# Kernel optimization log

Measured on AMD Instinct MI355X. Metric: run time of the kernel, lower is better.

## Reference

```python
import jax, jax.numpy as jnp
import numpy as np

EPS = 1e-5
INC1, INC2 = 256, 256
MIDC1, MIDC2 = INC1 // 4, INC2 // 4  # 64, 64
B, H, W = 4, 64, 64


def _bn_eval(x, w, b, m, v):
    # x: (B, C, H, W); inference-mode BatchNorm2d
    inv = w / jnp.sqrt(v + EPS)
    return x * inv[None, :, None, None] + (b - m * inv)[None, :, None, None]


def setup_inputs() -> dict:
    key = jax.random.key(0)
    ks = jax.random.split(key, 24)
    f32 = jnp.float32
    d = {
        'fusion': jax.random.normal(ks[0], (B, INC1, H, W), f32),
        'input_rgb': jax.random.normal(ks[1], (B, INC1, H, W), f32),
        'input_dsm': jax.random.normal(ks[2], (B, INC2, H, W), f32),
        # BatchNorm2d params (eval mode: running stats)
        'bn1_w': jax.random.normal(ks[3], (INC1,), f32) * 0.1 + 1.0,
        'bn1_b': jax.random.normal(ks[4], (INC1,), f32) * 0.1,
        'bn1_m': jax.random.normal(ks[5], (INC1,), f32) * 0.1,
        'bn1_v': jax.random.uniform(ks[6], (INC1,), f32, 0.5, 1.5),
        'bn2_w': jax.random.normal(ks[7], (INC2,), f32) * 0.1 + 1.0,
        'bn2_b': jax.random.normal(ks[8], (INC2,), f32) * 0.1,
        'bn2_m': jax.random.normal(ks[9], (INC2,), f32) * 0.1,
        'bn2_v': jax.random.uniform(ks[10], (INC2,), f32, 0.5, 1.5),
        # Linear layers: weight is (out, in) like torch
        'kq1_w': jax.random.normal(ks[11], (2 * MIDC2, INC1), f32) * 0.02,
        'kq1_b': jnp.zeros((2 * MIDC2,), f32),
        'kq2_w': jax.random.normal(ks[12], (2 * MIDC2, INC2), f32) * 0.02,
        'kq2_b': jnp.zeros((2 * MIDC2,), f32),
        'v_w': jax.random.normal(ks[13], (2 * MIDC1, INC1), f32) * 0.02,
        'v_b': jnp.zeros((2 * MIDC1,), f32),
        'out_w': jax.random.normal(ks[14], (INC1, 2 * MIDC1), f32) * 0.02,
        'out_b': jnp.zeros((INC1,), f32),
        'bnl_w': jax.random.normal(ks[15], (INC1,), f32) * 0.1 + 1.0,
        'bnl_b': jax.random.normal(ks[16], (INC1,), f32) * 0.1,
        'bnl_m': jax.random.normal(ks[17], (INC1,), f32) * 0.1,
        'bnl_v': jax.random.uniform(ks[18], (INC1,), f32, 0.5, 1.5),
        'gamma': jax.random.normal(ks[19], (1,), f32) * 0.1,
    }
    return d


def reference(fusion, input_rgb, input_dsm,
              bn1_w, bn1_b, bn1_m, bn1_v,
              bn2_w, bn2_b, bn2_m, bn2_v,
              kq1_w, kq1_b, kq2_w, kq2_b,
              v_w, v_b, out_w, out_b,
              bnl_w, bnl_b, bnl_m, bnl_v, gamma):
    b, _, h, w = fusion.shape
    N = h * w
    rgb = _bn_eval(input_rgb, bn1_w, bn1_b, bn1_m, bn1_v)
    dsm = _bn_eval(input_dsm, bn2_w, bn2_b, bn2_m, bn2_v)
    # flatten NCHW -> (B, N, C)
    rgb_t = rgb.transpose(0, 2, 3, 1).reshape(b, N, -1)
    dsm_t = dsm.transpose(0, 2, 3, 1).reshape(b, N, -1)
    kq1 = rgb_t @ kq1_w.T + kq1_b  # (B, N, 2*MIDC2)
    kq2 = dsm_t @ kq2_w.T + kq2_b  # (B, N, 2*MIDC2)
    # channel shuffle with groups=2: interleave kq1/kq2 channels
    kq = jnp.stack([kq1, kq2], axis=-1).reshape(b, N, 4 * MIDC2)
    k1 = kq[..., 0 * MIDC2:1 * MIDC2]
    q1 = kq[..., 1 * MIDC2:2 * MIDC2]
    k2 = kq[..., 2 * MIDC2:3 * MIDC2]
    q2 = kq[..., 3 * MIDC2:4 * MIDC2]
    fus_t = fusion.transpose(0, 2, 3, 1).reshape(b, N, -1)
    vproj = fus_t @ v_w.T + v_b  # (B, N, 2*MIDC1)
    v1 = vproj[..., :MIDC1]
    v2 = vproj[..., MIDC1:]
    scale = 1.0 / jnp.sqrt(jnp.float32(MIDC2))
    # branch 1: naive softmax attention (dropout is identity at eval)
    a1 = jax.nn.softmax(jnp.einsum('bnd,bmd->bnm', q1, k1) * scale, axis=-1)
    o1 = jnp.einsum('bnm,bmd->bnd', a1, v1)
    # branch 2
    a2 = jax.nn.softmax(jnp.einsum('bnd,bmd->bnm', q2, k2) * scale, axis=-1)
    o2 = jnp.einsum('bnm,bmd->bnd', a2, v2)
    o = jnp.concatenate([o1, o2], axis=-1).reshape(b, h, w, 2 * MIDC1)
    o = o @ out_w.T + out_b  # (B, H, W, INC1)
    o = o.transpose(0, 3, 1, 2)  # (B, INC1, H, W)
    o = _bn_eval(o, bnl_w, bnl_b, bnl_m, bnl_v)
    out = jax.nn.sigmoid(o) * fusion * gamma + fusion
    return out
```

## Files before the change

kernel.cpp:

```cpp
#include <hip/hip_runtime.h>

typedef __bf16 bf16;
typedef __bf16 bf16x8 __attribute__((ext_vector_type(8)));
typedef float f32x2 __attribute__((ext_vector_type(2)));
typedef float f32x4 __attribute__((ext_vector_type(4)));
typedef float f32x16 __attribute__((ext_vector_type(16)));
typedef unsigned int u32;
typedef u32 u32x2 __attribute__((ext_vector_type(2)));
typedef u32 u32x4 __attribute__((ext_vector_type(4)));

#define MFMA16(A,B,C) __builtin_amdgcn_mfma_f32_16x16x32_bf16(A,B,C,0,0,0)
#define MFMA32(A,B,C) __builtin_amdgcn_mfma_f32_32x32x16_bf16(A,B,C,0,0,0)

#define ALPHA 0.18033688f
#define LOG2E 1.44269504f

static __device__ __forceinline__ u32 cvt_pk_bf16(float lo, float hi) {
    u32 r;
    asm("v_cvt_pk_bf16_f32 %0, %1, %2" : "=v"(r) : "v"(lo), "v"(hi));
    return r;
}
static __device__ __forceinline__ void permlane32_swap(u32& a, u32& b) {
    asm("v_permlane32_swap_b32 %0, %1" : "+v"(a), "+v"(b));
}
static __device__ __forceinline__ float vexp2(float x) {
    float r;
    asm("v_exp_f32 %0, %1" : "=v"(r) : "v"(x));
    return r;
}
static __device__ __forceinline__ float vrcp(float x) {
    float r;
    asm("v_rcp_f32 %0, %1" : "=v"(r) : "v"(x));
    return r;
}
static __device__ __forceinline__ void stage16(const bf16* g, bf16* l) {
    __builtin_amdgcn_global_load_lds(
        (const __attribute__((address_space(1))) void*)g,
        (__attribute__((address_space(3))) void*)l, 16, 0, 0);
}

__global__ __launch_bounds__(64) void wprep_kernel(
    const float* __restrict__ kq1w, const float* __restrict__ kq1b,
    const float* __restrict__ bn1w, const float* __restrict__ bn1b,
    const float* __restrict__ bn1m, const float* __restrict__ bn1v,
    const float* __restrict__ kq2w, const float* __restrict__ kq2b,
    const float* __restrict__ bn2w, const float* __restrict__ bn2b,
    const float* __restrict__ bn2m, const float* __restrict__ bn2v,
    const float* __restrict__ vw,   const float* __restrict__ vb,
    const float* __restrict__ outw, const float* __restrict__ outb,
    const float* __restrict__ bnlw, const float* __restrict__ bnlb,
    const float* __restrict__ bnlm, const float* __restrict__ bnlv,
    bf16* __restrict__ Wk1, bf16* __restrict__ Wk2, bf16* __restrict__ Wv,
    bf16* __restrict__ Wo,
    float* __restrict__ B1, float* __restrict__ B2, float* __restrict__ Bv,
    float* __restrict__ Bo)
{
    const int blk = blockIdx.x, lane = threadIdx.x;
    if (blk < 384) {
        const int arr = blk >> 7, j = blk & 127;
        const float* W  = arr == 0 ? kq1w : arr == 1 ? kq2w : vw;
        const float* bs = arr == 0 ? kq1b : arr == 1 ? kq2b : vb;
        bf16*  Wd = arr == 0 ? Wk1 : arr == 1 ? Wk2 : Wv;
        float* Bd = arr == 0 ? B1  : arr == 1 ? B2  : Bv;
        const float scale = (arr < 2 && ((j >> 5) & 1)) ? ALPHA : 1.0f;
        const int c0 = lane * 4;
        f32x4 w4 = *(const f32x4*)(W + j * 256 + c0);
        f32x4 o4; float dot = 0.f;
        if (arr < 2) {
            const float* bw = arr ? bn2w : bn1w;
            const float* bb = arr ? bn2b : bn1b;
            const float* bm = arr ? bn2m : bn1m;
            const float* bv = arr ? bn2v : bn1v;
            f32x4 gw = *(const f32x4*)(bw + c0), gb = *(const f32x4*)(bb + c0);
            f32x4 gm = *(const f32x4*)(bm + c0), gv = *(const f32x4*)(bv + c0);
#pragma unroll
            for (int k = 0; k < 4; ++k) {
                float iv = gw[k] * rsqrtf(gv[k] + 1e-5f);
                float beta = gb[k] - gm[k] * iv;
                o4[k] = w4[k] * iv * scale;
                dot += w4[k] * beta;
            }
        } else {
#pragma unroll
            for (int k = 0; k < 4; ++k) o4[k] = w4[k];
        }
        u32x2 pk; pk[0] = cvt_pk_bf16(o4[0], o4[1]); pk[1] = cvt_pk_bf16(o4[2], o4[3]);
        *(u32x2*)(Wd + j * 256 + c0) = pk;
#pragma unroll
        for (int off = 32; off >= 1; off >>= 1) dot += __shfl_xor(dot, off);
        if (lane == 0) Bd[j] = (bs[j] + dot) * scale;
    } else {
        const int c = blk - 384;
        const float iv = bnlw[c] * rsqrtf(bnlv[c] + 1e-5f);
        const int k0 = lane * 2;
        f32x2 w2 = *(const f32x2*)(outw + c * 128 + k0);
        *(u32*)(Wo + c * 128 + k0) = cvt_pk_bf16(w2[0] * iv, w2[1] * iv);
        if (lane == 0) Bo[c] = outb[c] * iv + bnlb[c] - bnlm[c] * iv;
    }
}

__global__ __launch_bounds__(256) void prep_kernel(
    const float* __restrict__ rgb, const float* __restrict__ dsm,
    const float* __restrict__ fus,
    const bf16* __restrict__ Wk1, const bf16* __restrict__ Wk2,
    const bf16* __restrict__ Wv,
    const float* __restrict__ B1, const float* __restrict__ B2,
    const float* __restrict__ Bv,
    bf16* __restrict__ Kp, bf16* __restrict__ Q, bf16* __restrict__ Vp)
{
    __shared__ __align__(16) float sX[256][34];

    const int id = blockIdx.x;
    const int mode = id >> 9, sub = id & 511;
    const int b = sub >> 7, nt = sub & 127;
    const int t = threadIdx.x;

    const float* X  = mode == 0 ? rgb : mode == 1 ? dsm : fus;
    const bf16*  W  = mode == 0 ? Wk1 : mode == 1 ? Wk2 : Wv;
    const float* Bs = mode == 0 ? B1  : mode == 1 ? B2  : Bv;

    const float* Xb = X + (size_t)b * 1048576 + (size_t)nt * 32;

#pragma unroll
    for (int i = 0; i < 8; ++i) {
        const int chunk = i * 256 + t;
        const int c = chunk >> 3, nn4 = (chunk & 7) * 4;
        const f32x4 v4 = *(const f32x4*)(Xb + (size_t)c * 4096 + nn4);
        *(f32x4*)(&sX[c][nn4]) = v4;
    }
    __syncthreads();

    const int lane = t & 63, w = t >> 6;
    const int l15 = lane & 15, g = lane >> 4;
    const int nloc = (w & 1) * 16 + l15;
    const int n = nt * 32 + nloc;
    const int cibase = (w >> 1) * 4;

    const f32x4 z4 = {0.f, 0.f, 0.f, 0.f};
    f32x4 acc[4] = {z4, z4, z4, z4};

#pragma unroll
    for (int ks = 0; ks < 8; ++ks) {
        const int c0 = ks * 32 + g * 8;
        u32x4 xb;
#pragma unroll
        for (int pr = 0; pr < 4; ++pr)
            xb[pr] = cvt_pk_bf16(sX[c0 + 2 * pr][nloc], sX[c0 + 2 * pr + 1][nloc]);
        const bf16x8 bfr = __builtin_bit_cast(bf16x8, xb);
#pragma unroll
        for (int ci = 0; ci < 4; ++ci) {
            bf16x8 af = *(const bf16x8*)(W + ((cibase + ci) * 16 + l15) * 256 + c0);
            acc[ci] = MFMA16(af, bfr, acc[ci]);
        }
    }

#pragma unroll
    for (int ci = 0; ci < 4; ++ci) {
        const int cia = cibase + ci;
        const int j0 = cia * 16 + g * 4;
        const f32x4 bq = *(const f32x4*)(Bs + j0);
        float v0 = acc[ci][0] + bq[0], v1 = acc[ci][1] + bq[1];
        float v2 = acc[ci][2] + bq[2], v3 = acc[ci][3] + bq[3];
        if (mode == 2) {
            const int head = cia >> 2;
            const int bh = b * 2 + head;
            const int dbase = (cia & 3) * 16 + g * 4;
            const int kbg = n >> 6, key = n & 63;
            const int kc = key >> 4, hi2 = (key >> 3) & 1, inner = key & 7;
            bf16* vp = Vp + (size_t)(bh * 64 + kbg) * 4096;
            const float vv[4] = {v0, v1, v2, v3};
#pragma unroll
            for (int rr = 0; rr < 4; ++rr) {
                const int d = dbase + rr;
                const int chunk = (((d >> 5) * 4 + kc) * 2 + hi2) * 32 + (d & 31);
                vp[chunk * 8 + inner] = (bf16)vv[rr];
            }
        } else {
            const int seg = cia >> 1;
            const int head = seg >> 1;
            const int bh = b * 2 + head;
            const int d0 = (cia & 1) * 16 + g * 4 + (mode == 1 ? 32 : 0);
            u32x2 pk; pk[0] = cvt_pk_bf16(v0, v1); pk[1] = cvt_pk_bf16(v2, v3);
            if (seg & 1) {
                *(u32x2*)(Q + ((size_t)bh * 4096 + n) * 64 + d0) = pk;
            } else {
                const int kbg = n >> 6, r = n & 63;
                const int chunk = (((r >> 5) * 4 + (d0 >> 4)) * 2 + ((d0 >> 3) & 1)) * 32 + (r & 31);
                *(u32x2*)(Kp + (size_t)(bh * 64 + kbg) * 4096 + chunk * 8 + (d0 & 7)) = pk;
            }
        }
    }
}

__global__ __launch_bounds__(512) void attn_kernel(
    const bf16* __restrict__ Kp, const bf16* __restrict__ Q,
    const bf16* __restrict__ Vp,
    bf16* __restrict__ Opart, float* __restrict__ Ml)
{
    __shared__ __align__(16) bf16 sK[2][4096];
    __shared__ __align__(16) bf16 sV[2][4096];

    const int id = blockIdx.x;
    const int bh = id & 7;
    const int qt = (id >> 3) & 15;
    const int s  = id >> 7;

    const int t = threadIdx.x, lane = t & 63, w = t >> 6;
    const int l31 = lane & 31, hi = lane >> 5;
    const int qrow = qt * 256 + w * 32 + l31;
    const int base = bh * 4096;

    bf16x8 qf[4];
    {
        const bf16* qp = Q + ((size_t)(base + qrow)) * 64 + hi * 8;
#pragma unroll
        for (int ds = 0; ds < 4; ++ds) qf[ds] = *(const bf16x8*)(qp + ds * 16);
    }

    f32x16 ot0, ot1;
#pragma unroll
    for (int i = 0; i < 16; ++i) { ot0[i] = 0.f; ot1[i] = 0.f; }
    float lsum = 0.f;

    const bf16* Kblk = Kp + (size_t)(bh * 64 + s * 16) * 4096;
    const bf16* Vblk = Vp + (size_t)(bh * 64 + s * 16) * 4096;
    const int wo = w * 512 + lane * 8;

#define STAGE(BUF, KBI)                                                      \
    {                                                                        \
        const size_t gb = (size_t)(KBI) * 4096 + wo;                         \
        stage16(Kblk + gb, &sK[BUF][w * 512]);                               \
        stage16(Vblk + gb, &sV[BUF][w * 512]);                               \
    }

    STAGE(0, 0);
    __syncthreads();
    int buf = 0;

    for (int kb = 0; kb < 16; ++kb) {
        if (kb + 1 < 16) {
            if (buf) STAGE(0, kb + 1) else STAGE(1, kb + 1);
        }
        const bf16* Kl = &sK[buf][0];
        const bf16* Vl = &sV[buf][0];

        bf16x8 pa[4];
#pragma unroll
        for (int kt = 0; kt < 2; ++kt) {
            f32x16 a;
#pragma unroll
            for (int i = 0; i < 16; ++i) a[i] = 0.f;
#pragma unroll
            for (int ds = 0; ds < 4; ++ds)
                a = MFMA32(*(const bf16x8*)(Kl + (kt * 4 + ds) * 512 + lane * 8), qf[ds], a);
#pragma unroll
            for (int r = 0; r < 16; ++r) a[r] = vexp2(a[r]);
            lsum += (((a[0] + a[1]) + (a[2] + a[3])) +
                     ((a[4] + a[5]) + (a[6] + a[7]))) +
                    (((a[8] + a[9]) + (a[10] + a[11])) +
                     ((a[12] + a[13]) + (a[14] + a[15])));
            u32 wa0 = cvt_pk_bf16(a[0], a[1]);
            u32 wa1 = cvt_pk_bf16(a[2], a[3]);
            u32 wb0 = cvt_pk_bf16(a[4], a[5]);
            u32 wb1 = cvt_pk_bf16(a[6], a[7]);
            permlane32_swap(wa0, wb0);
            permlane32_swap(wa1, wb1);
            u32x4 pk0; pk0[0] = wa0; pk0[1] = wa1; pk0[2] = wb0; pk0[3] = wb1;
            pa[2 * kt] = __builtin_bit_cast(bf16x8, pk0);
            u32 wc0 = cvt_pk_bf16(a[8], a[9]);
            u32 wc1 = cvt_pk_bf16(a[10], a[11]);
            u32 wd0 = cvt_pk_bf16(a[12], a[13]);
            u32 wd1 = cvt_pk_bf16(a[14], a[15]);
            permlane32_swap(wc0, wd0);
            permlane32_swap(wc1, wd1);
            u32x4 pk1; pk1[0] = wc0; pk1[1] = wc1; pk1[2] = wd0; pk1[3] = wd1;
            pa[2 * kt + 1] = __builtin_bit_cast(bf16x8, pk1);
        }
#pragma unroll
        for (int ks = 0; ks < 4; ++ks)
            ot0 = MFMA32(*(const bf16x8*)(Vl + ks * 512 + lane * 8), pa[ks], ot0);
#pragma unroll
        for (int ks = 0; ks < 4; ++ks)
            ot1 = MFMA32(*(const bf16x8*)(Vl + (4 + ks) * 512 + lane * 8), pa[ks], ot1);
        __syncthreads();
        buf ^= 1;
    }
#undef STAGE

    const float lt = lsum + __shfl_xor(lsum, 32);

    const int row = base + qrow;
    bf16* op = Opart + ((size_t)s * 32768 + row) * 64;
#pragma unroll
    for (int a4 = 0; a4 < 4; ++a4) {
        u32x2 p0, p1;
        p0[0] = cvt_pk_bf16(ot0[a4 * 4 + 0], ot0[a4 * 4 + 1]);
        p0[1] = cvt_pk_bf16(ot0[a4 * 4 + 2], ot0[a4 * 4 + 3]);
        *(u32x2*)(op + a4 * 8 + hi * 4) = p0;
        p1[0] = cvt_pk_bf16(ot1[a4 * 4 + 0], ot1[a4 * 4 + 1]);
        p1[1] = cvt_pk_bf16(ot1[a4 * 4 + 2], ot1[a4 * 4 + 3]);
        *(u32x2*)(op + 32 + a4 * 8 + hi * 4) = p1;
    }
    Ml[(size_t)s * 32768 + row] = lt;
}

__global__ __launch_bounds__(256) void out_kernel(
    const bf16* __restrict__ Opart, const float* __restrict__ Ml,
    const bf16* __restrict__ Wo, const float* __restrict__ Bo,
    const float* __restrict__ fus, const float* __restrict__ gamma,
    float* __restrict__ out)
{
    __shared__ __align__(16) bf16 sO[4 * 2 * 16 * 72];

    const int id = blockIdx.x;
    const int b = id >> 8, nt = id & 255;
    const int t = threadIdx.x, lane = t & 63, w = t >> 6;
    const int l15 = lane & 15, g = lane >> 4;
    const int n = nt * 16 + l15;
    const int cibase = w * 4;

    for (int chunk = t; chunk < 1152; chunk += 256) {
        const int s = chunk >> 8, rem = chunk & 255;
        const int h = rem >> 7, nl = (rem >> 3) & 15, d16 = chunk & 7;
        const size_t grow = (size_t)s * 32768 + (size_t)(b * 2 + h) * 4096 + nt * 16 + nl;
        const u32x4 v = *(const u32x4*)(Opart + grow * 64 + d16 * 8);
        *(u32x4*)(&sO[(((s * 2 + h) * 16 + nl) * 72) + d16 * 8]) = v;
    }
    __syncthreads();

    float rl[2];
#pragma unroll
    for (int h = 0; h < 2; ++h) {
        const int row = (b * 2 + h) * 4096 + n;
        float L = 0.f;
#pragma unroll
        for (int s = 0; s < 4; ++s) L += Ml[(size_t)s * 32768 + row];
        rl[h] = vrcp(L);
    }

    const f32x4 z4 = {0.f, 0.f, 0.f, 0.f};
    f32x4 acc[4] = {z4, z4, z4, z4};
#pragma unroll
    for (int ks = 0; ks < 4; ++ks) {
        const int h = ks >> 1;
        const int kk = (ks & 1) * 32 + g * 8;
        float fc[8] = {0.f, 0.f, 0.f, 0.f, 0.f, 0.f, 0.f, 0.f};
#pragma unroll
        for (int s = 0; s < 4; ++s) {
            const u32x4 pv = *(const u32x4*)(&sO[(((s * 2 + h) * 16 + l15) * 72) + kk]);
#pragma unroll
            for (int pj = 0; pj < 4; ++pj) {
                fc[2 * pj]     += __builtin_bit_cast(float, pv[pj] << 16);
                fc[2 * pj + 1] += __builtin_bit_cast(float, pv[pj] & 0xffff0000u);
            }
        }
        u32x4 pb_;
#pragma unroll
        for (int pj = 0; pj < 4; ++pj)
            pb_[pj] = cvt_pk_bf16(fc[2 * pj] * rl[h], fc[2 * pj + 1] * rl[h]);
        const bf16x8 bfr = __builtin_bit_cast(bf16x8, pb_);
        const int k0 = ks * 32 + g * 8;
#pragma unroll
        for (int ci = 0; ci < 4; ++ci) {
            bf16x8 af = *(const bf16x8*)(Wo + ((cibase + ci) * 16 + l15) * 128 + k0);
            acc[ci] = MFMA16(af, bfr, acc[ci]);
        }
    }
    const float gam = gamma[0];
#pragma unroll
    for (int ci = 0; ci < 4; ++ci) {
        const int c0 = (cibase + ci) * 16 + g * 4;
        const f32x4 bo = *(const f32x4*)(Bo + c0);
#pragma unroll
        for (int r = 0; r < 4; ++r) {
            const int c = c0 + r;
            const size_t off = ((size_t)(b * 256 + c)) * 4096 + n;
            const float v = acc[ci][r] + bo[r];
            const float sg = vrcp(1.0f + vexp2(-v * LOG2E));
            out[off] = fus[off] * fmaf(sg, gam, 1.0f);
        }
    }
}

extern "C" void kernel_launch(void* const* d_in, const int* in_sizes, int n_in,
                              void* d_out, int out_size, void* d_ws, size_t ws_size,
                              hipStream_t stream)
{
    (void)in_sizes; (void)n_in; (void)out_size; (void)ws_size;
    const float* fusion = (const float*)d_in[0];
    const float* rgb    = (const float*)d_in[1];
    const float* dsm    = (const float*)d_in[2];
    const float* bn1w = (const float*)d_in[3];
    const float* bn1b = (const float*)d_in[4];
    const float* bn1m = (const float*)d_in[5];
    const float* bn1v = (const float*)d_in[6];
    const float* bn2w = (const float*)d_in[7];
    const float* bn2b = (const float*)d_in[8];
    const float* bn2m = (const float*)d_in[9];
    const float* bn2v = (const float*)d_in[10];
    const float* kq1w = (const float*)d_in[11];
    const float* kq1b = (const float*)d_in[12];
    const float* kq2w = (const float*)d_in[13];
    const float* kq2b = (const float*)d_in[14];
    const float* vw   = (const float*)d_in[15];
    const float* vb   = (const float*)d_in[16];
    const float* outw = (const float*)d_in[17];
    const float* outb = (const float*)d_in[18];
    const float* bnlw = (const float*)d_in[19];
    const float* bnlb = (const float*)d_in[20];
    const float* bnlm = (const float*)d_in[21];
    const float* bnlv = (const float*)d_in[22];
    const float* gamma = (const float*)d_in[23];

    char* ws = (char*)d_ws;
    size_t off = 0;
    auto alloc = [&](size_t bytes) { char* p = ws + off; off = (off + bytes + 255) & ~(size_t)255; return p; };
    bf16* Wk1 = (bf16*)alloc(128 * 256 * 2);
    bf16* Wk2 = (bf16*)alloc(128 * 256 * 2);
    bf16* Wv  = (bf16*)alloc(128 * 256 * 2);
    bf16* Wo  = (bf16*)alloc(256 * 128 * 2);
    float* B1 = (float*)alloc(128 * 4);
    float* B2 = (float*)alloc(128 * 4);
    float* Bv = (float*)alloc(128 * 4);
    float* Bo = (float*)alloc(256 * 4);
    bf16* Kp    = (bf16*)alloc((size_t)8 * 64 * 4096 * 2);
    bf16* Q     = (bf16*)alloc((size_t)8 * 4096 * 64 * 2);
    bf16* Vp    = (bf16*)alloc((size_t)8 * 64 * 4096 * 2);
    bf16* Opart = (bf16*)alloc((size_t)4 * 8 * 4096 * 64 * 2);
    float* Ml   = (float*)alloc((size_t)4 * 8 * 4096 * 4);

    wprep_kernel<<<640, 64, 0, stream>>>(
        kq1w, kq1b, bn1w, bn1b, bn1m, bn1v,
        kq2w, kq2b, bn2w, bn2b, bn2m, bn2v,
        vw, vb, outw, outb, bnlw, bnlb, bnlm, bnlv,
        Wk1, Wk2, Wv, Wo, B1, B2, Bv, Bo);
    prep_kernel<<<1536, 256, 0, stream>>>(rgb, dsm, fusion,
        Wk1, Wk2, Wv, B1, B2, Bv, Kp, Q, Vp);
    attn_kernel<<<512, 512, 0, stream>>>(Kp, Q, Vp, Opart, Ml);
    out_kernel<<<1024, 256, 0, stream>>>(Opart, Ml, Wo, Bo, fusion, gamma, (float*)d_out);
}
```

Measured before the change: 94.74 us.

## Process two 32-row query tiles per wave in attention kernel to reuse K/V fragments

The attention kernel now runs 4 waves per block instead of 8, and each wave handles 64 query rows as two 32-row tiles. Each K and V fragment read from LDS then feeds two MFMAs, which halves LDS read traffic per unit of work and gives more independent MFMA chains for latency hiding. Staging is spread over fewer threads with two loads each. The cost is higher register pressure (four output accumulators plus two score tiles) and fewer waves per block, which may reduce occupancy.

```diff
diff --git a/kernel.cpp b/kernel.cpp
--- a/kernel.cpp
+++ b/kernel.cpp
@@ -192,7 +192,7 @@
     }
 }
 
-__global__ __launch_bounds__(512) void attn_kernel(
+__global__ __launch_bounds__(256) void attn_kernel(
     const bf16* __restrict__ Kp, const bf16* __restrict__ Q,
     const bf16* __restrict__ Vp,
     bf16* __restrict__ Opart, float* __restrict__ Ml)
@@ -207,30 +207,36 @@
 
     const int t = threadIdx.x, lane = t & 63, w = t >> 6;
     const int l31 = lane & 31, hi = lane >> 5;
-    const int qrow = qt * 256 + w * 32 + l31;
+    const int qbase = qt * 256 + w * 64;
     const int base = bh * 4096;
 
-    bf16x8 qf[4];
+    bf16x8 qf0[4], qf1[4];
     {
-        const bf16* qp = Q + ((size_t)(base + qrow)) * 64 + hi * 8;
-#pragma unroll
-        for (int ds = 0; ds < 4; ++ds) qf[ds] = *(const bf16x8*)(qp + ds * 16);
-    }
-
-    f32x16 ot0, ot1;
-#pragma unroll
-    for (int i = 0; i < 16; ++i) { ot0[i] = 0.f; ot1[i] = 0.f; }
-    float lsum = 0.f;
+        const bf16* qp0 = Q + ((size_t)(base + qbase + l31)) * 64 + hi * 8;
+        const bf16* qp1 = qp0 + 32 * 64;
+#pragma unroll
+        for (int ds = 0; ds < 4; ++ds) {
+            qf0[ds] = *(const bf16x8*)(qp0 + ds * 16);
+            qf1[ds] = *(const bf16x8*)(qp1 + ds * 16);
+        }
+    }
+
+    f32x16 ot00, ot01, ot10, ot11;
+#pragma unroll
+    for (int i = 0; i < 16; ++i) { ot00[i] = 0.f; ot01[i] = 0.f; ot10[i] = 0.f; ot11[i] = 0.f; }
+    float ls0 = 0.f, ls1 = 0.f;
 
     const bf16* Kblk = Kp + (size_t)(bh * 64 + s * 16) * 4096;
     const bf16* Vblk = Vp + (size_t)(bh * 64 + s * 16) * 4096;
-    const int wo = w * 512 + lane * 8;
+    const int wo = t * 8;
 
 #define STAGE(BUF, KBI)                                                      \
     {                                                                        \
         const size_t gb = (size_t)(KBI) * 4096 + wo;                         \
-        stage16(Kblk + gb, &sK[BUF][w * 512]);                               \
-        stage16(Vblk + gb, &sV[BUF][w * 512]);                               \
+        stage16(Kblk + gb,        &sK[BUF][w * 512]);                        \
+        stage16(Kblk + gb + 2048, &sK[BUF][w * 512 + 2048]);                 \
+        stage16(Vblk + gb,        &sV[BUF][w * 512]);                        \
+        stage16(Vblk + gb + 2048, &sV[BUF][w * 512 + 2048]);                 \
     }
 
     STAGE(0, 0);
@@ -244,64 +250,111 @@
         const bf16* Kl = &sK[buf][0];
         const bf16* Vl = &sV[buf][0];
 
-        bf16x8 pa[4];
 #pragma unroll
         for (int kt = 0; kt < 2; ++kt) {
-            f32x16 a;
-#pragma unroll
-            for (int i = 0; i < 16; ++i) a[i] = 0.f;
-#pragma unroll
-            for (int ds = 0; ds < 4; ++ds)
-                a = MFMA32(*(const bf16x8*)(Kl + (kt * 4 + ds) * 512 + lane * 8), qf[ds], a);
-#pragma unroll
-            for (int r = 0; r < 16; ++r) a[r] = vexp2(a[r]);
-            lsum += (((a[0] + a[1]) + (a[2] + a[3])) +
-                     ((a[4] + a[5]) + (a[6] + a[7]))) +
-                    (((a[8] + a[9]) + (a[10] + a[11])) +
-                     ((a[12] + a[13]) + (a[14] + a[15])));
-            u32 wa0 = cvt_pk_bf16(a[0], a[1]);
-            u32 wa1 = cvt_pk_bf16(a[2], a[3]);
-            u32 wb0 = cvt_pk_bf16(a[4], a[5]);
-            u32 wb1 = cvt_pk_bf16(a[6], a[7]);
-            permlane32_swap(wa0, wb0);
-            permlane32_swap(wa1, wb1);
-            u32x4 pk0; pk0[0] = wa0; pk0[1] = wa1; pk0[2] = wb0; pk0[3] = wb1;
-            pa[2 * kt] = __builtin_bit_cast(bf16x8, pk0);
-            u32 wc0 = cvt_pk_bf16(a[8], a[9]);
-            u32 wc1 = cvt_pk_bf16(a[10], a[11]);
-            u32 wd0 = cvt_pk_bf16(a[12], a[13]);
-            u32 wd1 = cvt_pk_bf16(a[14], a[15]);
-            permlane32_swap(wc0, wd0);
-            permlane32_swap(wc1, wd1);
-            u32x4 pk1; pk1[0] = wc0; pk1[1] = wc1; pk1[2] = wd0; pk1[3] = wd1;
-            pa[2 * kt + 1] = __builtin_bit_cast(bf16x8, pk1);
-        }
-#pragma unroll
-        for (int ks = 0; ks < 4; ++ks)
-            ot0 = MFMA32(*(const bf16x8*)(Vl + ks * 512 + lane * 8), pa[ks], ot0);
-#pragma unroll
-        for (int ks = 0; ks < 4; ++ks)
-            ot1 = MFMA32(*(const bf16x8*)(Vl + (4 + ks) * 512 + lane * 8), pa[ks], ot1);
+            f32x16 a0, a1;
+#pragma unroll
+            for (int i = 0; i < 16; ++i) { a0[i] = 0.f; a1[i] = 0.f; }
+#pragma unroll
+            for (int ds = 0; ds < 4; ++ds) {
+                const bf16x8 kf = *(const bf16x8*)(Kl + (kt * 4 + ds) * 512 + lane * 8);
+                a0 = MFMA32(kf, qf0[ds], a0);
+                a1 = MFMA32(kf, qf1[ds], a1);
+            }
+#pragma unroll
+            for (int r = 0; r < 16; ++r) a0[r] = vexp2(a0[r]);
+            ls0 += (((a0[0] + a0[1]) + (a0[2] + a0[3])) +
+                    ((a0[4] + a0[5]) + (a0[6] + a0[7]))) +
+                   (((a0[8] + a0[9]) + (a0[10] + a0[11])) +
+                    ((a0[12] + a0[13]) + (a0[14] + a0[15])));
+#pragma unroll
+            for (int r = 0; r < 16; ++r) a1[r] = vexp2(a1[r]);
+            ls1 += (((a1[0] + a1[1]) + (a1[2] + a1[3])) +
+                    ((a1[4] + a1[5]) + (a1[6] + a1[7]))) +
+                   (((a1[8] + a1[9]) + (a1[10] + a1[11])) +
+                    ((a1[12] + a1[13]) + (a1[14] + a1[15])));
+            bf16x8 paA0, paB0, paA1, paB1;
+            {
+                u32 wa0 = cvt_pk_bf16(a0[0], a0[1]);
+                u32 wa1 = cvt_pk_bf16(a0[2], a0[3]);
+                u32 wb0 = cvt_pk_bf16(a0[4], a0[5]);
+                u32 wb1 = cvt_pk_bf16(a0[6], a0[7]);
+                permlane32_swap(wa0, wb0);
+                permlane32_swap(wa1, wb1);
+                u32x4 pk0; pk0[0] = wa0; pk0[1] = wa1; pk0[2] = wb0; pk0[3] = wb1;
+                paA0 = __builtin_bit_cast(bf16x8, pk0);
+                u32 wc0 = cvt_pk_bf16(a0[8], a0[9]);
+                u32 wc1 = cvt_pk_bf16(a0[10], a0[11]);
+                u32 wd0 = cvt_pk_bf16(a0[12], a0[13]);
+                u32 wd1 = cvt_pk_bf16(a0[14], a0[15]);
+                permlane32_swap(wc0, wd0);
+                permlane32_swap(wc1, wd1);
+                u32x4 pk1; pk1[0] = wc0; pk1[1] = wc1; pk1[2] = wd0; pk1[3] = wd1;
+                paB0 = __builtin_bit_cast(bf16x8, pk1);
+            }
+            {
+                u32 wa0 = cvt_pk_bf16(a1[0], a1[1]);
+                u32 wa1 = cvt_pk_bf16(a1[2], a1[3]);
+                u32 wb0 = cvt_pk_bf16(a1[4], a1[5]);
+                u32 wb1 = cvt_pk_bf16(a1[6], a1[7]);
+                permlane32_swap(wa0, wb0);
+                permlane32_swap(wa1, wb1);
+                u32x4 pk0; pk0[0] = wa0; pk0[1] = wa1; pk0[2] = wb0; pk0[3] = wb1;
+                paA1 = __builtin_bit_cast(bf16x8, pk0);
+                u32 wc0 = cvt_pk_bf16(a1[8], a1[9]);
+                u32 wc1 = cvt_pk_bf16(a1[10], a1[11]);
+                u32 wd0 = cvt_pk_bf16(a1[12], a1[13]);
+                u32 wd1 = cvt_pk_bf16(a1[14], a1[15]);
+                permlane32_swap(wc0, wd0);
+                permlane32_swap(wc1, wd1);
+                u32x4 pk1; pk1[0] = wc0; pk1[1] = wc1; pk1[2] = wd0; pk1[3] = wd1;
+                paB1 = __builtin_bit_cast(bf16x8, pk1);
+            }
+            {
+                const int ks = 2 * kt;
+                const bf16x8 v0 = *(const bf16x8*)(Vl + ks * 512 + lane * 8);
+                const bf16x8 v1 = *(const bf16x8*)(Vl + (4 + ks) * 512 + lane * 8);
+                ot00 = MFMA32(v0, paA0, ot00);
+                ot01 = MFMA32(v1, paA0, ot01);
+                ot10 = MFMA32(v0, paA1, ot10);
+                ot11 = MFMA32(v1, paA1, ot11);
+            }
+            {
+                const int ks = 2 * kt + 1;
+                const bf16x8 v0 = *(const bf16x8*)(Vl + ks * 512 + lane * 8);
+                const bf16x8 v1 = *(const bf16x8*)(Vl + (4 + ks) * 512 + lane * 8);
+                ot00 = MFMA32(v0, paB0, ot00);
+                ot01 = MFMA32(v1, paB0, ot01);
+                ot10 = MFMA32(v0, paB1, ot10);
+                ot11 = MFMA32(v1, paB1, ot11);
+            }
+        }
         __syncthreads();
         buf ^= 1;
     }
 #undef STAGE
 
-    const float lt = lsum + __shfl_xor(lsum, 32);
-
-    const int row = base + qrow;
-    bf16* op = Opart + ((size_t)s * 32768 + row) * 64;
-#pragma unroll
-    for (int a4 = 0; a4 < 4; ++a4) {
-        u32x2 p0, p1;
-        p0[0] = cvt_pk_bf16(ot0[a4 * 4 + 0], ot0[a4 * 4 + 1]);
-        p0[1] = cvt_pk_bf16(ot0[a4 * 4 + 2], ot0[a4 * 4 + 3]);
-        *(u32x2*)(op + a4 * 8 + hi * 4) = p0;
-        p1[0] = cvt_pk_bf16(ot1[a4 * 4 + 0], ot1[a4 * 4 + 1]);
-        p1[1] = cvt_pk_bf16(ot1[a4 * 4 + 2], ot1[a4 * 4 + 3]);
-        *(u32x2*)(op + 32 + a4 * 8 + hi * 4) = p1;
-    }
-    Ml[(size_t)s * 32768 + row] = lt;
+    const float lt0 = ls0 + __shfl_xor(ls0, 32);
+    const float lt1 = ls1 + __shfl_xor(ls1, 32);
+
+#pragma unroll
+    for (int ti = 0; ti < 2; ++ti) {
+        const int row = base + qbase + ti * 32 + l31;
+        bf16* op = Opart + ((size_t)s * 32768 + row) * 64;
+        const f32x16& d0 = ti ? ot10 : ot00;
+        const f32x16& d1 = ti ? ot11 : ot01;
+#pragma unroll
+        for (int a4 = 0; a4 < 4; ++a4) {
+            u32x2 p0, p1;
+            p0[0] = cvt_pk_bf16(d0[a4 * 4 + 0], d0[a4 * 4 + 1]);
+            p0[1] = cvt_pk_bf16(d0[a4 * 4 + 2], d0[a4 * 4 + 3]);
+            *(u32x2*)(op + a4 * 8 + hi * 4) = p0;
+            p1[0] = cvt_pk_bf16(d1[a4 * 4 + 0], d1[a4 * 4 + 1]);
+            p1[1] = cvt_pk_bf16(d1[a4 * 4 + 2], d1[a4 * 4 + 3]);
+            *(u32x2*)(op + 32 + a4 * 8 + hi * 4) = p1;
+        }
+        Ml[(size_t)s * 32768 + row] = ti ? lt1 : lt0;
+    }
 }
 
 __global__ __launch_bounds__(256) void out_kernel(
@@ -436,6 +489,6 @@
         Wk1, Wk2, Wv, Wo, B1, B2, Bv, Bo);
     prep_kernel<<<1536, 256, 0, stream>>>(rgb, dsm, fusion,
         Wk1, Wk2, Wv, B1, B2, Bv, Kp, Q, Vp);
-    attn_kernel<<<512, 512, 0, stream>>>(Kp, Q, Vp, Opart, Ml);
+    attn_kernel<<<512, 256, 0, stream>>>(Kp, Q, Vp, Opart, Ml);
     out_kernel<<<1024, 256, 0, stream>>>(Opart, Ml, Wo, Bo, fusion, gamma, (float*)d_out);
 }
```

New measurement: 97.31 us. 1.03x slower.
